# Performance work log

Measured on AMD Instinct MI355X. Metric: run time of the kernel, lower is better.

Reference implementation:

```python
import jax, jax.numpy as jnp
import numpy as np

B, T_TREES, LEAVES = 1024, 34, 16
E = 128            # entity = logic = theorem embedding size
N_NF, N_LF = 4, 3  # binary numerical / logic function experts
V_ENT, V_TH = 2000, 32
GT_MAX, ENT_MAX, TH_MAX = 8, 16, 8


def setup_inputs() -> dict:
    key = jax.random.key(0)
    ks = jax.random.split(key, 24)
    s2e = 1.0 / np.sqrt(2 * E)
    s4e = 1.0 / np.sqrt(4 * E)
    se = 1.0 / np.sqrt(E)
    inp = {
        'leaf_idx': jax.random.randint(ks[0], (B, T_TREES, LEAVES), 0, V_ENT),
        'nf_ids':   jax.random.randint(ks[1], (B, T_TREES, 15), 0, N_NF),
        'lf_ids':   jax.random.randint(ks[2], (B, GT_MAX + 1), 0, N_LF),
        'th_idx':   jax.random.randint(ks[3], (B, TH_MAX), 0, V_TH),
        'ent_emb':  jax.random.normal(ks[4], (V_ENT, E)) * 0.02,
        'th_emb':   jax.random.normal(ks[5], (V_TH, E)) * 0.02,
        # nf two2one expert MLPs: Linear(2E,2E) -> ReLU -> Linear(2E,E)
        'nf_W1': jax.random.normal(ks[6], (N_NF, 2 * E, 2 * E)) * s2e,
        'nf_b1': jnp.zeros((N_NF, 2 * E)),
        'nf_W2': jax.random.normal(ks[7], (N_NF, 2 * E, E)) * s2e,
        'nf_b2': jnp.zeros((N_NF, E)),
        # lf two2one expert MLPs: Linear(2E,4E) -> ReLU -> Linear(4E,E)
        'lf_W1': jax.random.normal(ks[8], (N_LF, 2 * E, 4 * E)) * s2e,
        'lf_b1': jnp.zeros((N_LF, 4 * E)),
        'lf_W2': jax.random.normal(ks[9], (N_LF, 4 * E, E)) * s4e,
        'lf_b2': jnp.zeros((N_LF, E)),
        # higher attention linears: logic_size -> {entity,entity,theorem} size
        'he_W': jax.random.normal(ks[10], (E, E)) * se, 'he_b': jnp.zeros((E,)),
        'hg_W': jax.random.normal(ks[11], (E, E)) * se, 'hg_b': jnp.zeros((E,)),
        'ht_W': jax.random.normal(ks[12], (E, E)) * se, 'ht_b': jnp.zeros((E,)),
    }
    return inp


def _expert_mlp(x, ids, W1, b1, W2, b2):
    # x: [..., Din], ids: [...] selecting among K experts; masked sum over K (small fixed loop)
    out = jnp.zeros(x.shape[:-1] + (W2.shape[-1],), x.dtype)
    for k in range(W1.shape[0]):
        h = jax.nn.relu(x @ W1[k] + b1[k]) @ W2[k] + b2[k]
        out = out + jnp.where((ids == k)[..., None], h, 0.0)
    return out


def _attend(keys, q):
    # keys: [B, N, D], q: [B, D] -> attentive context [B, D]
    a = jax.nn.softmax(jnp.einsum('bnd,bd->bn', keys, q), axis=-1)
    return jnp.einsum('bn,bnd->bd', a, keys)


def _forward(leaf_idx, nf_ids, lf_ids, th_idx, ent_emb, th_emb,
             nf_W1, nf_b1, nf_W2, nf_b2, lf_W1, lf_b1, lf_W2, lf_b2,
             he_W, he_b, hg_W, hg_b, ht_W, ht_b):
    # leaf entity embedding lookup: [B, 34, 16, E]
    cur = ent_emb[leaf_idx]
    # recursive tree reduction over 4 levels of binary nf MLPs (batched over all nodes)
    off = 0
    for lvl in range(4):
        n = LEAVES >> (lvl + 1)  # nodes at this level: 8,4,2,1
        x = cur.reshape(cur.shape[0], T_TREES, n, 2 * E)  # concat(left,right)
        ids = nf_ids[..., off:off + n]
        off += n
        cur = _expert_mlp(x, ids, nf_W1, nf_b1, nf_W2, nf_b2)
    roots = cur[..., 0, :]                       # [B, 34, E]
    ent = roots[:, :ENT_MAX]                     # [B, 16, E] standalone entities
    pairs = roots[:, ENT_MAX:].reshape(roots.shape[0], GT_MAX + 1, 2 * E)
    stmt = _expert_mlp(pairs, lf_ids, lf_W1, lf_b1, lf_W2, lf_b2)  # [B, 9, E]
    gt = stmt[:, :GT_MAX]                        # [B, 8, E] ground truths
    obj = stmt[:, GT_MAX]                        # [B, E]    objective
    th = th_emb[th_idx]                          # [B, 8, E] theorems
    ent_ctx = _attend(ent, obj @ he_W + he_b)
    gt_ctx = _attend(gt, obj @ hg_W + hg_b)
    th_ctx = _attend(th, obj @ ht_W + ht_b)
    # higher attentive state: 2*L + E + T = 512
    return jnp.concatenate([obj, gt_ctx, ent_ctx, th_ctx], axis=-1)


def reference(leaf_idx, nf_ids, lf_ids, th_idx, ent_emb, th_emb,
              nf_W1, nf_b1, nf_W2, nf_b2, lf_W1, lf_b1, lf_W2, lf_b2,
              he_W, he_b, hg_W, hg_b, ht_W, ht_b):
    return _forward(leaf_idx, nf_ids, lf_ids, th_idx, ent_emb, th_emb,
                    nf_W1, nf_b1, nf_W2, nf_b2, lf_W1, lf_b1, lf_W2, lf_b2,
                    he_W, he_b, hg_W, hg_b, ht_W, ht_b)
```

## Files before the change

kernel.cpp:

```cpp
#include <hip/hip_runtime.h>
#include <math.h>


typedef unsigned short u16;
typedef unsigned int   u32;
typedef unsigned long long u64;
typedef __attribute__((ext_vector_type(8))) short v8s;
typedef __attribute__((ext_vector_type(4))) float f32x4;

__device__ __forceinline__ float b2f(u16 u) { return __uint_as_float(((u32)u) << 16); }
__device__ __forceinline__ u16 f2b(float f) {
  f = (f == f) ? f : 0.f;
  u32 x = __float_as_uint(f);
  u32 r = x + 0x7fffu + ((x >> 16) & 1u);
  return (u16)(r >> 16);
}

#define NTREE 34816
#define RLEAF 9216


__global__ __launch_bounds__(256) void perm_hist_k(
    const int* __restrict__ nf, int* __restrict__ bh,
    const int CB, const int bt0, const int nb)
{
  const int gid = blockIdx.x * 256 + threadIdx.x;
  int id = -1, lr = 0, cofs = 12, ioff = 14, shift = 0;
  if (gid < 8 * CB)       { lr = gid;          cofs = 0;  ioff = 0;  shift = 3; }
  else if (gid < 12 * CB) { lr = gid - 8*CB;   cofs = 4;  ioff = 8;  shift = 2; }
  else if (gid < 14 * CB) { lr = gid - 12*CB;  cofs = 8;  ioff = 12; shift = 1; }
  else if (gid < 15 * CB) { lr = gid - 14*CB;          }
  if (gid < 15 * CB) {
    int bt = bt0 + (lr >> shift);
    int n  = lr & ((1 << shift) - 1);
    id = nf[bt * 15 + ioff + n];
  }
  __shared__ int lcnt[16];
  if (threadIdx.x < 16) lcnt[threadIdx.x] = 0;
  __syncthreads();
  const int lane = threadIdx.x & 63;
  #pragma unroll
  for (int e = 0; e < 4; ++e) {
    u64 m = __ballot(id == e);
    if (m && lane == __builtin_ctzll(m))
      atomicAdd(&lcnt[cofs + e], (int)__popcll(m));
  }
  __syncthreads();
  if (threadIdx.x < 16)
    bh[threadIdx.x * nb + blockIdx.x] = lcnt[threadIdx.x];
}

__global__ __launch_bounds__(1024) void perm_scan_k(
    int* __restrict__ bh, int* __restrict__ cnt, const int nb)
{
  const int s = threadIdx.x >> 6;
  const int lane = threadIdx.x & 63;
  int carry = 0;
  for (int b0 = 0; b0 < nb; b0 += 64) {
    const int b = b0 + lane;
    int v = (b < nb) ? bh[s * nb + b] : 0;
    int x = v;
    #pragma unroll
    for (int d = 1; d < 64; d <<= 1) {
      int y = __shfl_up(x, d);
      if (lane >= d) x += y;
    }
    if (b < nb) bh[s * nb + b] = carry + x - v;
    carry += __shfl(x, 63);
  }
  if (lane == 0) cnt[s] = carry;
}

__global__ __launch_bounds__(256) void perm_scatter_k(
    const int* __restrict__ nf, const int* __restrict__ bh,
    int* __restrict__ perm, const int CB, const int bt0, const int nb)
{
  const int gid = blockIdx.x * 256 + threadIdx.x;
  int id = -1, lr = 0, rows = CB, cofs = 12, pofs = 56 * CB, ioff = 14, shift = 0;
  if (gid < 8 * CB)       { lr = gid;          rows = 8*CB; cofs = 0;  pofs = 0;      ioff = 0;  shift = 3; }
  else if (gid < 12 * CB) { lr = gid - 8*CB;   rows = 4*CB; cofs = 4;  pofs = 32*CB;  ioff = 8;  shift = 2; }
  else if (gid < 14 * CB) { lr = gid - 12*CB;  rows = 2*CB; cofs = 8;  pofs = 48*CB;  ioff = 12; shift = 1; }
  else if (gid < 15 * CB) { lr = gid - 14*CB;                 }
  if (gid < 15 * CB) {
    int bt = bt0 + (lr >> shift);
    int n  = lr & ((1 << shift) - 1);
    id = nf[bt * 15 + ioff + n];
  }
  __shared__ int wc[4][16];
  const int w = threadIdx.x >> 6, lane = threadIdx.x & 63;
  if (lane < 16) wc[w][lane] = 0;
  __syncthreads();
  u64 msave[4];
  #pragma unroll
  for (int e = 0; e < 4; ++e) {
    u64 m = __ballot(id == e);
    msave[e] = m;
    if (m && lane == __builtin_ctzll(m))
      wc[w][cofs + e] = (int)__popcll(m);
  }
  __syncthreads();
  #pragma unroll
  for (int e = 0; e < 4; ++e) {
    if (id == e) {
      const int slot = cofs + e;
      int base = bh[slot * nb + blockIdx.x];
      #pragma unroll
      for (int w2 = 0; w2 < 3; ++w2)
        if (w2 < w) base += wc[w2][slot];
      perm[pofs + e * rows + base +
           (int)__popcll(msave[e] & ((1ull << lane) - 1ull))] = lr;
    }
  }
}

__global__ __launch_bounds__(256) void leaf_perm_k(
    const int* __restrict__ lf, int* __restrict__ cnt, int* __restrict__ perm)
{
  const int gid = blockIdx.x * 256 + threadIdx.x;
  const int id = lf[gid];
  const int lane = threadIdx.x & 63;
  for (int e = 0; e < 3; ++e) {
    u64 m = __ballot(id == e);
    if (!m) continue;
    int leader = __builtin_ctzll(m);
    int bp = 0;
    if (lane == leader) bp = atomicAdd(&cnt[e], (int)__popcll(m));
    bp = __shfl(bp, leader);
    if (id == e)
      perm[e * RLEAF + bp + (int)__popcll(m & ((1ull << lane) - 1ull))] = gid;
  }
}

__global__ __launch_bounds__(256) void transpose_k(
    const float* __restrict__ s0, const float* __restrict__ s1,
    const float* __restrict__ s2, const float* __restrict__ s3,
    const float* __restrict__ s4,
    u16* __restrict__ d0, u16* __restrict__ d1, u16* __restrict__ d2,
    u16* __restrict__ d3, u16* __restrict__ d4)
{
  int idx = blockIdx.x * 256 + threadIdx.x;
  if (idx < 262144) {
    int t = idx;
    int blk = t >> 9, w9 = t & 511, ln = w9 >> 3, j = w9 & 7;
    int kt = blk & 7, mt = (blk >> 3) & 15, e = blk >> 7;
    int o = mt * 16 + (ln & 15);
    int k = kt * 32 + (ln >> 4) * 8 + j;
    d0[t] = f2b(s0[(e << 16) + (k << 8) + o]);
  } else if (idx < 393216) {
    int t = idx - 262144;
    int blk = t >> 9, w9 = t & 511, ln = w9 >> 3, j = w9 & 7;
    int kt = blk & 7, mt = (blk >> 3) & 7, e = blk >> 6;
    int o = mt * 16 + (ln & 15);
    int k = kt * 32 + (ln >> 4) * 8 + j;
    d1[t] = f2b(s1[(e << 15) + (k << 7) + o]);
  } else if (idx < 786432) {
    int t = idx - 393216;
    int blk = t >> 9, w9 = t & 511, ln = w9 >> 3, j = w9 & 7;
    int kt = blk & 7, mt = (blk >> 3) & 31, e = blk >> 8;
    int o = mt * 16 + (ln & 15);
    int k = kt * 32 + (ln >> 4) * 8 + j;
    d2[t] = f2b(s2[(e << 17) + (k << 9) + o]);
  } else if (idx < 983040) {
    int t = idx - 786432;
    int blk = t >> 9, w9 = t & 511, ln = w9 >> 3, j = w9 & 7;
    int kt = blk & 15, mt = (blk >> 4) & 7, e = blk >> 7;
    int o = mt * 16 + (ln & 15);
    int k = kt * 32 + (ln >> 4) * 8 + j;
    d3[t] = f2b(s3[(e << 16) + (k << 7) + o]);
  } else if (idx < 1239040) {
    int t = idx - 983040;
    d4[t] = f2b(s4[t]);
  }
}

template<int HID, int NEXP, int MODE, int MR>
__global__ __launch_bounds__(256, 2) void mlp_k(
    const u16* __restrict__ src, const int* __restrict__ lidx,
    const u16* __restrict__ emb,
    const int* __restrict__ perm, const int* __restrict__ cnt,
    const int rows, const int bt0,
    const u16* __restrict__ W1f, const float* __restrict__ b1,
    const u16* __restrict__ W2f, const float* __restrict__ b2,
    u16* __restrict__ dst)
{
  constexpr int NT  = MR / 16;
  constexpr int MT1 = HID / 64;
  constexpr int K2  = HID / 32;
  constexpr bool PREF1 = (MT1 <= 4);
  constexpr int XB  = MR * 512;
  constexpr int HB  = MR * HID * 2;
  constexpr int UB  = XB > HB ? XB : HB;
  __shared__ __align__(16) char uni[UB];
  __shared__ int prc[MR], rid[MR], soff[2 * MR];
  u16* const xs = (u16*)uni;
  u16* const hs = (u16*)uni;

  int bin = -1, tile = 0, cb = 0;
  {
    int rem = blockIdx.x;
    #pragma unroll
    for (int e = 0; e < NEXP; ++e) {
      int ce = cnt[e];
      int tt = (ce + MR - 1) / MR;
      if (bin < 0) {
        if (rem < tt) { bin = e; tile = rem; cb = ce; }
        else rem -= tt;
      }
    }
  }
  if (bin < 0) return;
  const int rbase = tile * MR;
  const int tid = threadIdx.x;
  const int w  = tid >> 6;
  const int lane = tid & 63;
  const int lm = lane & 15;
  const int lq = lane >> 4;

  const u16* const W1b = W1f + ((size_t)(bin * (HID / 16) + w * MT1) << 12) + lane * 8;
  const u16* const W2b = W2f + ((size_t)((bin * 8 + w * 2) * K2) << 9) + lane * 8;

  v8s afb[2][PREF1 ? MT1 : 1];
  if (PREF1) {
    #pragma unroll
    for (int m = 0; m < MT1; ++m)
      afb[0][m] = *(const v8s*)(W1b + (size_t)(m * 8) * 512);
  }

  if (tid < MR) {
    int rl = rbase + tid;
    int rlc = rl < cb ? rl : (cb - 1);
    rlc = rlc < 0 ? 0 : rlc;
    int rc = perm[(size_t)bin * rows + rlc];
    rc = rc < 0 ? 0 : (rc >= rows ? rows - 1 : rc);
    prc[tid] = rc;
    rid[tid] = (rl < cb) ? rc : -1;
  }
  __syncthreads();

  int rdn[NT];
  #pragma unroll
  for (int n = 0; n < NT; ++n) rdn[n] = rid[n * 16 + lm];

  if (MODE == 0) {
    if (tid < 2 * MR) {
      int r = tid >> 1, h = tid & 1;
      int rc = prc[r];
      int bt = bt0 + (rc >> 3), node = rc & 7;
      int ix = lidx[bt * 16 + node * 2 + h];
      ix = ix < 0 ? 0 : (ix > 1999 ? 1999 : ix);
      soff[tid] = ix * 256;
    }
  } else {
    if (tid < MR) {
      int rc = prc[tid];
      int base;
      if (MODE == 1) base = rc * 512;
      else { int bq = rc / 9, g = rc - bq * 9; base = (bq * 34 + 16 + 2 * g) * 256; }
      soff[2 * tid]     = base;
      soff[2 * tid + 1] = base + 256;
    }
  }
  __syncthreads();

  const char* const sb = (MODE == 0) ? (const char*)emb : (const char*)src;
  #pragma unroll
  for (int i = 0; i < MR / 8; ++i) {
    int c = i * 256 + tid;
    int seg = c >> 4, sub = c & 15;
    uint4 v = *(const uint4*)(sb + (size_t)(u32)soff[seg] + sub * 16);
    int r = seg >> 1;
    int c32 = ((seg & 1) << 4) + sub;
    int cs = c32 ^ ((r & 7) << 1);
    *(uint4*)(uni + r * 512 + cs * 16) = v;
  }
  __syncthreads();

  f32x4 acc[MT1][NT];
  #pragma unroll
  for (int m = 0; m < MT1; ++m)
    #pragma unroll
    for (int n = 0; n < NT; ++n)
      acc[m][n] = f32x4{0.f, 0.f, 0.f, 0.f};

  if (PREF1) {
    #pragma unroll
    for (int k = 0; k < 8; ++k) {
      const int cur = k & 1, nxt = cur ^ 1;
      if (k < 7)
        #pragma unroll
        for (int m = 0; m < MT1; ++m)
          afb[nxt][m] = *(const v8s*)(W1b + (size_t)(m * 8 + k + 1) * 512);
      v8s bfr[NT];
      #pragma unroll
      for (int n = 0; n < NT; ++n) {
        int r = n * 16 + lm;
        int cs = (k * 4 + lq) ^ ((lm & 7) << 1);
        bfr[n] = *(const v8s*)(xs + r * 256 + cs * 8);
      }
      #pragma unroll
      for (int m = 0; m < MT1; ++m)
        #pragma unroll
        for (int n = 0; n < NT; ++n)
          acc[m][n] = __builtin_amdgcn_mfma_f32_16x16x32_bf16(afb[cur][m], bfr[n], acc[m][n], 0, 0, 0);
    }
  } else {
    #pragma unroll
    for (int k = 0; k < 8; ++k) {
      v8s bfr[NT];
      #pragma unroll
      for (int n = 0; n < NT; ++n) {
        int r = n * 16 + lm;
        int cs = (k * 4 + lq) ^ ((lm & 7) << 1);
        bfr[n] = *(const v8s*)(xs + r * 256 + cs * 8);
      }
      #pragma unroll
      for (int m = 0; m < MT1; ++m) {
        const v8s af = *(const v8s*)(W1b + (size_t)(m * 8 + k) * 512);
        #pragma unroll
        for (int n = 0; n < NT; ++n)
          acc[m][n] = __builtin_amdgcn_mfma_f32_16x16x32_bf16(af, bfr[n], acc[m][n], 0, 0, 0);
      }
    }
  }

  v8s afb2[2][2];
  #pragma unroll
  for (int m = 0; m < 2; ++m)
    afb2[0][m] = *(const v8s*)(W2b + (size_t)(m * K2) * 512);

  __syncthreads();

  const float* b1b = b1 + bin * HID;
  #pragma unroll
  for (int m = 0; m < MT1; ++m) {
    const int f = (w * MT1 + m) * 16 + lq * 4;
    float bb0 = b1b[f], bb1 = b1b[f + 1], bb2 = b1b[f + 2], bb3 = b1b[f + 3];
    #pragma unroll
    for (int n = 0; n < NT; ++n) {
      union { u16 h[4]; uint2 v; } pk;
      f32x4 a = acc[m][n];
      pk.h[0] = f2b(fmaxf(a.x + bb0, 0.f));
      pk.h[1] = f2b(fmaxf(a.y + bb1, 0.f));
      pk.h[2] = f2b(fmaxf(a.z + bb2, 0.f));
      pk.h[3] = f2b(fmaxf(a.w + bb3, 0.f));
      int r = n * 16 + lm;
      int cs = (f >> 3) ^ ((lm & 7) << 1);
      *(uint2*)(uni + (size_t)r * (HID * 2) + (cs << 4) + (f & 7) * 2) = pk.v;
    }
  }
  __syncthreads();

  f32x4 acc2[2][NT];
  #pragma unroll
  for (int m = 0; m < 2; ++m)
    #pragma unroll
    for (int n = 0; n < NT; ++n)
      acc2[m][n] = f32x4{0.f, 0.f, 0.f, 0.f};

  #pragma unroll
  for (int k = 0; k < K2; ++k) {
    const int cur = k & 1, nxt = cur ^ 1;
    if (k < K2 - 1)
      #pragma unroll
      for (int m = 0; m < 2; ++m)
        afb2[nxt][m] = *(const v8s*)(W2b + (size_t)(m * K2 + k + 1) * 512);
    v8s bfr[NT];
    #pragma unroll
    for (int n = 0; n < NT; ++n) {
      int r = n * 16 + lm;
      int cs = (k * 4 + lq) ^ ((lm & 7) << 1);
      bfr[n] = *(const v8s*)(hs + (size_t)r * HID + cs * 8);
    }
    #pragma unroll
    for (int m = 0; m < 2; ++m)
      #pragma unroll
      for (int n = 0; n < NT; ++n)
        acc2[m][n] = __builtin_amdgcn_mfma_f32_16x16x32_bf16(afb2[cur][m], bfr[n], acc2[m][n], 0, 0, 0);
  }
  const float* b2b = b2 + bin * 128;
  #pragma unroll
  for (int m = 0; m < 2; ++m) {
    const int f = (w * 2 + m) * 16 + lq * 4;
    float bb0 = b2b[f], bb1 = b2b[f + 1], bb2 = b2b[f + 2], bb3 = b2b[f + 3];
    #pragma unroll
    for (int n = 0; n < NT; ++n) {
      if (rdn[n] >= 0) {
        union { u16 h[4]; uint2 v; } pk;
        f32x4 a = acc2[m][n];
        pk.h[0] = f2b(a.x + bb0);
        pk.h[1] = f2b(a.y + bb1);
        pk.h[2] = f2b(a.z + bb2);
        pk.h[3] = f2b(a.w + bb3);
        *(uint2*)(dst + (size_t)rdn[n] * 128 + f) = pk.v;
      }
    }
  }
}

__global__ __launch_bounds__(128) void attn_k(
    const u16* __restrict__ stmt, const u16* __restrict__ roots,
    const float* __restrict__ themb, const int* __restrict__ thidx,
    const float* __restrict__ wHe, const float* __restrict__ bHe,
    const float* __restrict__ wHg, const float* __restrict__ bHg,
    const float* __restrict__ wHt, const float* __restrict__ bHt,
    float* __restrict__ out)
{
  const int b = blockIdx.x, t = threadIdx.x;
  __shared__ float obj_s[128], q_s[128], keys_s[16 * 132], a_s[16];

  const float obj = b2f(stmt[((size_t)b * 9 + 8) * 128 + t]);
  obj_s[t] = obj;
  out[(size_t)b * 512 + t] = obj;
  __syncthreads();

  for (int a = 0; a < 3; ++a) {
    int cntk;
    const float *Wt, *bv;
    if (a == 0) {
      cntk = 8; Wt = wHg; bv = bHg;
      for (int j = 0; j < 8; ++j)
        keys_s[j * 132 + t] = b2f(stmt[((size_t)b * 9 + j) * 128 + t]);
    } else if (a == 1) {
      cntk = 16; Wt = wHe; bv = bHe;
      for (int j = 0; j < 16; ++j)
        keys_s[j * 132 + t] = b2f(roots[((size_t)b * 34 + j) * 128 + t]);
    } else {
      cntk = 8; Wt = wHt; bv = bHt;
      for (int j = 0; j < 8; ++j) {
        int ti = thidx[b * 8 + j] & 31;
        keys_s[j * 132 + t] = themb[(size_t)ti * 128 + t];
      }
    }
    float qa = bv[t];
    for (int k = 0; k < 128; ++k) qa += obj_s[k] * Wt[k * 128 + t];
    q_s[t] = (qa == qa) ? qa : 0.f;
    __syncthreads();
    if (t < cntk) {
      float sc = 0.f;
      for (int k = 0; k < 128; ++k) sc += keys_s[t * 132 + k] * q_s[k];
      a_s[t] = (sc == sc) ? sc : 0.f;
    }
    __syncthreads();
    if (t == 0) {
      float mx = a_s[0];
      for (int j = 1; j < cntk; ++j) mx = fmaxf(mx, a_s[j]);
      float sm = 0.f;
      for (int j = 0; j < cntk; ++j) { float e = expf(a_s[j] - mx); a_s[j] = e; sm += e; }
      float inv = 1.f / sm;
      for (int j = 0; j < cntk; ++j) a_s[j] *= inv;
    }
    __syncthreads();
    float c = 0.f;
    for (int j = 0; j < cntk; ++j) c += a_s[j] * keys_s[j * 132 + t];
    out[(size_t)b * 512 + 128 * (a + 1) + t] = c;
    __syncthreads();
  }
}

extern "C" void kernel_launch(void* const* d_in, const int* in_sizes, int n_in,
                              void* d_out, int out_size, void* d_ws, size_t ws_size,
                              hipStream_t stream)
{
  const int*   leaf_idx = (const int*)d_in[0];
  const int*   nf_ids   = (const int*)d_in[1];
  const int*   lf_ids   = (const int*)d_in[2];
  const int*   th_idx   = (const int*)d_in[3];
  const float* ent_emb  = (const float*)d_in[4];
  const float* th_emb   = (const float*)d_in[5];
  const float* nf_W1 = (const float*)d_in[6];
  const float* nf_b1 = (const float*)d_in[7];
  const float* nf_W2 = (const float*)d_in[8];
  const float* nf_b2 = (const float*)d_in[9];
  const float* lf_W1 = (const float*)d_in[10];
  const float* lf_b1 = (const float*)d_in[11];
  const float* lf_W2 = (const float*)d_in[12];
  const float* lf_b2 = (const float*)d_in[13];
  const float* he_W = (const float*)d_in[14];
  const float* he_b = (const float*)d_in[15];
  const float* hg_W = (const float*)d_in[16];
  const float* hg_b = (const float*)d_in[17];
  const float* ht_W = (const float*)d_in[18];
  const float* ht_b = (const float*)d_in[19];

  int CB = NTREE;
  while (CB > 544 && 14500000ull + (unsigned long long)CB * 3320ull > (unsigned long long)ws_size)
    CB >>= 1;
  const int nch = NTREE / CB;
  const int NB = (15 * CB + 255) / 256;

  char* ws = (char*)d_ws;
  size_t off = 0;
  auto take = [&](size_t bytes) -> char* {
    char* p = ws + off;
    off = (off + bytes + 255) & ~(size_t)255;
    return p;
  };
  int* cnt      = (int*)take(8192);
  int* leafperm = (int*)take((size_t)3 * RLEAF * 4);
  int* chperm   = (int*)take((size_t)60 * CB * 4);
  int* bh       = (int*)take((size_t)16 * NB * 4);
  u16* wN1  = (u16*)take((size_t)4 * 256 * 256 * 2);
  u16* wN2  = (u16*)take((size_t)4 * 128 * 256 * 2);
  u16* wL1  = (u16*)take((size_t)3 * 512 * 256 * 2);
  u16* wL2  = (u16*)take((size_t)3 * 128 * 512 * 2);
  u16* embB = (u16*)take((size_t)2000 * 128 * 2);
  u16* bufA  = (u16*)take((size_t)CB * 8 * 128 * 2);
  u16* bufB  = (u16*)take((size_t)CB * 4 * 128 * 2);
  u16* roots = (u16*)take((size_t)NTREE * 128 * 2);
  u16* stmt  = (u16*)take((size_t)RLEAF * 128 * 2);

  int* leafcnt = cnt + nch * 16;

  hipMemsetAsync(cnt, 0, (size_t)(nch * 16 + 8) * 4, stream);
  transpose_k<<<4840, 256, 0, stream>>>(nf_W1, nf_W2, lf_W1, lf_W2, ent_emb,
                                        wN1, wN2, wL1, wL2, embB);
  leaf_perm_k<<<36, 256, 0, stream>>>(lf_ids, leafcnt, leafperm);

  for (int c = 0; c < nch; ++c) {
    const int bt0 = c * CB;
    int* ccnt = cnt + c * 16;
    perm_hist_k<<<NB, 256, 0, stream>>>(nf_ids, bh, CB, bt0, NB);
    perm_scan_k<<<1, 1024, 0, stream>>>(bh, ccnt, NB);
    perm_scatter_k<<<NB, 256, 0, stream>>>(nf_ids, bh, chperm, CB, bt0, NB);
    mlp_k<256, 4, 0, 64><<<CB / 8 + 4, 256, 0, stream>>>(
        nullptr, leaf_idx, embB, chperm, ccnt, 8 * CB, bt0,
        wN1, nf_b1, wN2, nf_b2, bufA);
    mlp_k<256, 4, 1, 64><<<CB / 16 + 4, 256, 0, stream>>>(
        bufA, nullptr, nullptr, chperm + 32 * CB, ccnt + 4, 4 * CB, 0,
        wN1, nf_b1, wN2, nf_b2, bufB);
    mlp_k<256, 4, 1, 64><<<CB / 32 + 4, 256, 0, stream>>>(
        bufB, nullptr, nullptr, chperm + 48 * CB, ccnt + 8, 2 * CB, 0,
        wN1, nf_b1, wN2, nf_b2, bufA);
    mlp_k<256, 4, 1, 64><<<(CB + 63) / 64 + 4, 256, 0, stream>>>(
        bufA, nullptr, nullptr, chperm + 56 * CB, ccnt + 12, CB, 0,
        wN1, nf_b1, wN2, nf_b2, roots + (size_t)bt0 * 128);
  }

  mlp_k<512, 3, 2, 32><<<RLEAF / 32 + 3, 256, 0, stream>>>(
      roots, nullptr, nullptr, leafperm, leafcnt, RLEAF, 0,
      wL1, lf_b1, wL2, lf_b2, stmt);

  attn_k<<<1024, 128, 0, stream>>>(stmt, roots, th_emb, th_idx,
                                   he_W, he_b, hg_W, hg_b, ht_W, ht_b,
                                   (float*)d_out);
}
```

Measured before the change: 363.9 us.

## Coalesce weight transpose via LDS tile and raise mlp_k occupancy hint

```diff
diff --git a/kernel.cpp b/kernel.cpp
--- a/kernel.cpp
+++ b/kernel.cpp
@@ -138,43 +138,36 @@
     u16* __restrict__ d0, u16* __restrict__ d1, u16* __restrict__ d2,
     u16* __restrict__ d3, u16* __restrict__ d4)
 {
-  int idx = blockIdx.x * 256 + threadIdx.x;
-  if (idx < 262144) {
-    int t = idx;
-    int blk = t >> 9, w9 = t & 511, ln = w9 >> 3, j = w9 & 7;
-    int kt = blk & 7, mt = (blk >> 3) & 15, e = blk >> 7;
-    int o = mt * 16 + (ln & 15);
-    int k = kt * 32 + (ln >> 4) * 8 + j;
-    d0[t] = f2b(s0[(e << 16) + (k << 8) + o]);
-  } else if (idx < 393216) {
-    int t = idx - 262144;
-    int blk = t >> 9, w9 = t & 511, ln = w9 >> 3, j = w9 & 7;
-    int kt = blk & 7, mt = (blk >> 3) & 7, e = blk >> 6;
-    int o = mt * 16 + (ln & 15);
-    int k = kt * 32 + (ln >> 4) * 8 + j;
-    d1[t] = f2b(s1[(e << 15) + (k << 7) + o]);
-  } else if (idx < 786432) {
-    int t = idx - 393216;
-    int blk = t >> 9, w9 = t & 511, ln = w9 >> 3, j = w9 & 7;
-    int kt = blk & 7, mt = (blk >> 3) & 31, e = blk >> 8;
-    int o = mt * 16 + (ln & 15);
-    int k = kt * 32 + (ln >> 4) * 8 + j;
-    d2[t] = f2b(s2[(e << 17) + (k << 9) + o]);
-  } else if (idx < 983040) {
-    int t = idx - 786432;
-    int blk = t >> 9, w9 = t & 511, ln = w9 >> 3, j = w9 & 7;
-    int kt = blk & 15, mt = (blk >> 4) & 7, e = blk >> 7;
-    int o = mt * 16 + (ln & 15);
-    int k = kt * 32 + (ln >> 4) * 8 + j;
-    d3[t] = f2b(s3[(e << 16) + (k << 7) + o]);
-  } else if (idx < 1239040) {
-    int t = idx - 983040;
-    d4[t] = f2b(s4[t]);
+  __shared__ float tile[16][17];
+  const int t = threadIdx.x;
+  const int idx0 = blockIdx.x * 256;
+  if (idx0 < 983040) {
+    const float* s; u16* d; int tb, estr, O, kt, mt, e;
+    int tloc0;
+    if (idx0 < 262144)      { s = s0; d = d0; tb = 0;      estr = 65536;  O = 256; }
+    else if (idx0 < 393216) { s = s1; d = d1; tb = 262144; estr = 32768;  O = 128; }
+    else if (idx0 < 786432) { s = s2; d = d2; tb = 393216; estr = 131072; O = 512; }
+    else                    { s = s3; d = d3; tb = 786432; estr = 65536;  O = 128; }
+    tloc0 = idx0 - tb;
+    const int blk = tloc0 >> 9;
+    const int hb  = (tloc0 >> 8) & 1;
+    if (idx0 < 262144)      { kt = blk & 7;  mt = (blk >> 3) & 15; e = blk >> 7; }
+    else if (idx0 < 393216) { kt = blk & 7;  mt = (blk >> 3) & 7;  e = blk >> 6; }
+    else if (idx0 < 786432) { kt = blk & 7;  mt = (blk >> 3) & 31; e = blk >> 8; }
+    else                    { kt = blk & 15; mt = (blk >> 4) & 7;  e = blk >> 7; }
+    const int o0 = mt * 16;
+    const int k0 = kt * 32 + hb * 16;
+    tile[t >> 4][t & 15] = s[(size_t)e * estr + (size_t)(k0 + (t >> 4)) * O + o0 + (t & 15)];
+    __syncthreads();
+    d[tloc0 + t] = f2b(tile[((t >> 7) << 3) + (t & 7)][(t >> 3) & 15]);
+  } else {
+    int tl = idx0 + t - 983040;
+    d4[tl] = f2b(s4[tl]);
   }
 }
 
 template<int HID, int NEXP, int MODE, int MR>
-__global__ __launch_bounds__(256, 2) void mlp_k(
+__global__ __launch_bounds__(256, 3) void mlp_k(
     const u16* __restrict__ src, const int* __restrict__ lidx,
     const u16* __restrict__ emb,
     const int* __restrict__ perm, const int* __restrict__ cnt,
```

Result: no change. 361.6 us (-0.6%).
